# Kernel optimization log

Measured on AMD Instinct MI355X. Metric: run time of the kernel, lower is better.

Reference implementation:

```python
import jax, jax.numpy as jnp
import numpy as np

B, CF, CG, CI = 2, 64, 64, 32
D = H = W = 64

def setup_inputs() -> dict:
    key = jax.random.key(0)
    k1, k2, k3, k4, k5 = jax.random.split(key, 5)
    x = jax.random.normal(k1, (B, CF, D, H, W), dtype=jnp.float32)
    g = jax.random.normal(k2, (B, CG, D, H, W), dtype=jnp.float32)
    # 1x1x1 conv weights reduce to [out_ch, in_ch]; kaiming-like scale
    Wg = jax.random.normal(k3, (CI, CG), dtype=jnp.float32) * (1.0 / np.sqrt(CG))
    Wx = jax.random.normal(k4, (CI, CF), dtype=jnp.float32) * (1.0 / np.sqrt(CF))
    Wpsi = jax.random.normal(k5, (1, CI), dtype=jnp.float32) * (1.0 / np.sqrt(CI))
    return {"x": x, "g": g, "Wg": Wg, "Wx": Wx, "Wpsi": Wpsi}

def reference(x, g, Wg, Wx, Wpsi):
    # 1x1x1 Conv3d == per-voxel matmul over channel dim
    g1 = jnp.einsum('oc,bcdhw->bodhw', Wg, g)          # [B,CI,D,H,W]
    x1 = jnp.einsum('oc,bcdhw->bodhw', Wx, x)          # [B,CI,D,H,W]
    a = jax.nn.relu(g1 + x1)
    psi = jnp.einsum('oc,bcdhw->bodhw', Wpsi, a)       # [B,1,D,H,W]
    psi = jax.nn.sigmoid(psi)
    return x * psi                                      # broadcast over CF
```

## Files before the change

kernel.cpp:

```cpp
#include <hip/hip_runtime.h>


#define SPAT 262144
#define NVOX 524288
#define CIN  64
#define COUT 32

__global__ __launch_bounds__(256) void transpose_w(const float* __restrict__ Wg,
                                                   const float* __restrict__ Wx,
                                                   float* __restrict__ Wcat) {
    int idx = blockIdx.x * 256 + threadIdx.x;
    int c = idx >> 6;
    int o = idx & 63;
    float v = (o < 32) ? Wg[o * CIN + c] : Wx[(o - 32) * CIN + c];
    Wcat[c * 64 + o] = v;
}

__global__ __launch_bounds__(256, 8) void gate_main(const float* __restrict__ x,
                                                    const float* __restrict__ g,
                                                    const float* __restrict__ Wcat,
                                                    const float* __restrict__ Wpsi,
                                                    float* __restrict__ out) {
    int p = blockIdx.x * 256 + threadIdx.x;
    int b = p >> 18;
    int s = p & (SPAT - 1);

    const float* __restrict__ xp = x + (size_t)b * CIN * SPAT + s;
    const float* __restrict__ gp = g + (size_t)b * CIN * SPAT + s;

    float acc[COUT];
#pragma unroll
    for (int o = 0; o < COUT; ++o) acc[o] = 0.0f;

#pragma unroll 4
    for (int c = 0; c < CIN; ++c) {
        float gc = __builtin_nontemporal_load(gp + (size_t)c * SPAT);
        float xc = xp[(size_t)c * SPAT];
        const float* w = Wcat + c * 64;
#pragma unroll
        for (int o = 0; o < COUT; ++o) {
            acc[o] = fmaf(w[o], gc, fmaf(w[32 + o], xc, acc[o]));
        }
    }

    float ps = 0.0f;
#pragma unroll
    for (int o = 0; o < COUT; ++o) {
        ps = fmaf(Wpsi[o], fmaxf(acc[o], 0.0f), ps);
    }
    float psi = 1.0f / (1.0f + __expf(-ps));

    float* __restrict__ op = out + (size_t)b * CIN * SPAT + s;
#pragma unroll 8
    for (int c = 0; c < CIN; ++c) {
        float xv = xp[(size_t)c * SPAT];
        __builtin_nontemporal_store(xv * psi, op + (size_t)c * SPAT);
    }
}

extern "C" void kernel_launch(void* const* d_in, const int* in_sizes, int n_in,
                              void* d_out, int out_size, void* d_ws, size_t ws_size,
                              hipStream_t stream) {
    const float* x    = (const float*)d_in[0];
    const float* g    = (const float*)d_in[1];
    const float* Wg   = (const float*)d_in[2];
    const float* Wx   = (const float*)d_in[3];
    const float* Wpsi = (const float*)d_in[4];
    float* out  = (float*)d_out;
    float* Wcat = (float*)d_ws;

    transpose_w<<<16, 256, 0, stream>>>(Wg, Wx, Wcat);
    gate_main<<<NVOX / 256, 256, 0, stream>>>(x, g, Wcat, Wpsi, out);
}
```

Baseline: 327.8 us.

## Double-buffer channel-group loads to prefetch next group during FMA compute

Splits the 64 input channels into groups of 8 and double-buffers the g and x loads in registers, issuing the next group's loads before computing FMAs on the current group. The aim is more memory-level parallelism per thread, so load latency is hidden in this bandwidth-bound kernel. The launch-bounds occupancy hint drops from 8 to 4 blocks per CU to make room for the extra registers, which reduces the latency hiding that came from having more waves resident.

After: 378.9 us. +15.6%, slower.

```diff
diff --git a/kernel.cpp b/kernel.cpp
--- a/kernel.cpp
+++ b/kernel.cpp
@@ -5,6 +5,8 @@
 #define NVOX 524288
 #define CIN  64
 #define COUT 32
+#define GRP  8
+#define NCG  (CIN / GRP)
 
 __global__ __launch_bounds__(256) void transpose_w(const float* __restrict__ Wg,
                                                    const float* __restrict__ Wx,
@@ -16,7 +18,7 @@
     Wcat[c * 64 + o] = v;
 }
 
-__global__ __launch_bounds__(256, 8) void gate_main(const float* __restrict__ x,
+__global__ __launch_bounds__(256, 4) void gate_main(const float* __restrict__ x,
                                                     const float* __restrict__ g,
                                                     const float* __restrict__ Wcat,
                                                     const float* __restrict__ Wpsi,
@@ -32,14 +34,50 @@
 #pragma unroll
     for (int o = 0; o < COUT; ++o) acc[o] = 0.0f;
 
-#pragma unroll 4
-    for (int c = 0; c < CIN; ++c) {
-        float gc = __builtin_nontemporal_load(gp + (size_t)c * SPAT);
-        float xc = xp[(size_t)c * SPAT];
-        const float* w = Wcat + c * 64;
+    float ga[GRP], xa[GRP], gb[GRP], xb[GRP];
+
 #pragma unroll
-        for (int o = 0; o < COUT; ++o) {
-            acc[o] = fmaf(w[o], gc, fmaf(w[32 + o], xc, acc[o]));
+    for (int k = 0; k < GRP; ++k) {
+        ga[k] = __builtin_nontemporal_load(gp + (size_t)k * SPAT);
+        xa[k] = xp[(size_t)k * SPAT];
+    }
+
+#pragma unroll 2
+    for (int cg = 0; cg < NCG; ++cg) {
+        if ((cg & 1) == 0) {
+            if (cg + 1 < NCG) {
+#pragma unroll
+                for (int k = 0; k < GRP; ++k) {
+                    int c = (cg + 1) * GRP + k;
+                    gb[k] = __builtin_nontemporal_load(gp + (size_t)c * SPAT);
+                    xb[k] = xp[(size_t)c * SPAT];
+                }
+            }
+#pragma unroll
+            for (int k = 0; k < GRP; ++k) {
+                int c = cg * GRP + k;
+                const float* w = Wcat + c * 64;
+#pragma unroll
+                for (int o = 0; o < COUT; ++o)
+                    acc[o] = fmaf(w[o], ga[k], fmaf(w[32 + o], xa[k], acc[o]));
+            }
+        } else {
+            if (cg + 1 < NCG) {
+#pragma unroll
+                for (int k = 0; k < GRP; ++k) {
+                    int c = (cg + 1) * GRP + k;
+                    ga[k] = __builtin_nontemporal_load(gp + (size_t)c * SPAT);
+                    xa[k] = xp[(size_t)c * SPAT];
+                }
+            }
+#pragma unroll
+            for (int k = 0; k < GRP; ++k) {
+                int c = cg * GRP + k;
+                const float* w = Wcat + c * 64;
+#pragma unroll
+                for (int o = 0; o < COUT; ++o)
+                    acc[o] = fmaf(w[o], gb[k], fmaf(w[32 + o], xb[k], acc[o]));
+            }
         }
     }
 
```
